# Optimization experiments

Hardware: AMD Instinct MI355X
Metric: run time of the kernel (lower is better)

## Reference

```python
import jax, jax.numpy as jnp
import numpy as np
import math

D = 128          # cfg.hiden_features_size
P0, P1 = 32, 32  # cfg.patch_size
T = 1.0          # default forward arg t


def _temporal_pe():
    # pe_k[i, :] = cat_j [sin(arg(t,i,j)), cos(arg(t,i,j))], i in [0,P1), j in [0,P0//2)
    i = jnp.arange(P1, dtype=jnp.float32)[:, None]          # [P1, 1]
    j = jnp.arange(P0 // 2, dtype=jnp.float32)[None, :]     # [1, P0//2]
    arg = T * jnp.pi * i / (1000.0 ** (2.0 * j / D))         # [P1, P0//2]
    pe = jnp.stack([jnp.sin(arg), jnp.cos(arg)], axis=-1)    # [P1, P0//2, 2]
    return pe.reshape(P1, P0)                                # [P1, P0]


def setup_inputs() -> dict:
    key = jax.random.key(0)
    kx, kw, kb = jax.random.split(key, 3)
    N, S = 128, P0 * P1
    x = jax.random.normal(kx, (N, S, D), dtype=jnp.float32)
    W = jax.random.normal(kw, (3 * D, D), dtype=jnp.float32) * (1.0 / math.sqrt(D))
    b = jax.random.normal(kb, (3 * D,), dtype=jnp.float32) * 0.01
    return {"x": x, "W": W, "b": b}


def reference(x, W, b):
    N, S, d = x.shape  # S = P0*P1, d = D
    # temporal positional encoding: multiply in spatial layout [N, P0, P1, d]
    pe = _temporal_pe()                                  # [P1, P0] (broadcast over x's [P0, P1])
    xs = x.reshape(N, P0, P1, d) * pe[None, :, :, None]
    xs = xs.reshape(N, S, d)
    # fused qkv projection: Linear(d, 3d)
    h = jnp.einsum('nsd,fd->nsf', xs, W) + b             # [N, S, 3d]
    # quirky split: view(N, S*d, 3) interleaves features in groups of 3
    qkv = h.reshape(N, S * d, 3)
    q, k, v = qkv[..., 0], qkv[..., 1], qkv[..., 2]      # each [N, S*d]
    # attention over the batch dimension: scores are [N, N]
    scores = (q @ k.T) / math.sqrt(d)
    attn = jax.nn.softmax(scores, axis=-1)
    return attn @ v                                      # [N, S*d]
```

## Files before the change

kernel.cpp:

```cpp
#include <hip/hip_runtime.h>
#include <math.h>

#define N_   128
#define S_   1024
#define D_   128
#define SD_  (S_ * D_)

#define WSP_PLANE 49152
#define NREP 16
#define SB   2
#define GRID_SC (S_ / SB)
#define QKP  36

typedef __attribute__((ext_vector_type(8))) short bf16x8;
typedef __attribute__((ext_vector_type(4))) short bf16x4;
typedef __attribute__((ext_vector_type(4))) float f32x4;
#define MFMA16 __builtin_amdgcn_mfma_f32_16x16x32_bf16

__device__ __forceinline__ float pe_scale(int s) {
    int i = s >> 5;
    int c = s & 31;
    double rexp = pow(1000.0, -(double)(c & ~1) / 128.0);
    double arg = M_PI * (double)i * rexp;
    return (float)((c & 1) ? cos(arg) : sin(arg));
}

__device__ __forceinline__ unsigned short bf16_rn(float f) {
    unsigned int u = __float_as_uint(f);
    u += 0x7fff + ((u >> 16) & 1);
    return (unsigned short)(u >> 16);
}
__device__ __forceinline__ float bf16_f(unsigned short h) {
    return __uint_as_float(((unsigned int)h) << 16);
}
__device__ __forceinline__ void split2(float f, unsigned short& h, unsigned short& l) {
    h = bf16_rn(f);
    l = bf16_rn(f - bf16_f(h));
}

__device__ __forceinline__ void load_split8(const float* p, float scale,
                                            bf16x8& hi, bf16x8& lo) {
    float4 u0 = *(const float4*)(p);
    float4 u1 = *(const float4*)(p + 4);
    unsigned short h[8], l[8];
    split2(u0.x * scale, h[0], l[0]); split2(u0.y * scale, h[1], l[1]);
    split2(u0.z * scale, h[2], l[2]); split2(u0.w * scale, h[3], l[3]);
    split2(u1.x * scale, h[4], l[4]); split2(u1.y * scale, h[5], l[5]);
    split2(u1.z * scale, h[6], l[6]); split2(u1.w * scale, h[7], l[7]);
    hi = bf16x8{(short)h[0],(short)h[1],(short)h[2],(short)h[3],
                (short)h[4],(short)h[5],(short)h[6],(short)h[7]};
    lo = bf16x8{(short)l[0],(short)l[1],(short)l[2],(short)l[3],
                (short)l[4],(short)l[5],(short)l[6],(short)l[7]};
}

__global__ __launch_bounds__(256) void k_prep(const float* __restrict__ W,
                                              unsigned short* __restrict__ Wsp,
                                              float* __restrict__ peT) {
    const int idx = blockIdx.x * 256 + threadIdx.x;
    if (idx < S_) peT[idx] = pe_scale(idx);
    const int rg = idx >> 7;
    const int d  = idx & 127;
    const int p  = rg % 3;
    const int r  = rg / 3;
    const int rc = r >> 5, m = r & 31;
    const int ks = d >> 5, quad = (d >> 3) & 3, j = d & 7;
    unsigned short h, l;
    split2(W[idx], h, l);
    const size_t off = (size_t)((((p * 4 + rc) * 4 + ks) * 4 + quad) * 32 + m) * 8 + j;
    Wsp[off] = h;
    Wsp[off + WSP_PLANE] = l;
}

__global__ __launch_bounds__(256, 2) void k_scores(const float* __restrict__ x,
                                                   const unsigned short* __restrict__ Wsp,
                                                   const float* __restrict__ b,
                                                   const float* __restrict__ peT,
                                                   float* __restrict__ sc,
                                                   int store_mode) {
    __shared__ unsigned short qk[2][4][128 * QKP];
    __shared__ float bl[384];

    const int t    = threadIdx.x;
    const int lane = t & 63;
    const int wv   = t >> 6;
    const int lid  = lane & 15;
    const int quad = lane >> 4;

    if (t < 128) { bl[t] = b[t]; bl[t + 128] = b[t + 128]; bl[t + 256] = b[t + 256]; }
    __syncthreads();

    const f32x4 fzero = {0.f, 0.f, 0.f, 0.f};
    f32x4 sacc[2][8];
#pragma unroll
    for (int i = 0; i < 2; ++i)
#pragma unroll
        for (int j = 0; j < 8; ++j) sacc[i][j] = fzero;

    for (int ss = 0; ss < SB; ++ss) {
        const int s = blockIdx.x * SB + ss;
        const float ps = peT[s];

        bf16x8 xh[2][4], xl[2][4];
#pragma unroll
        for (int nt = 0; nt < 2; ++nt) {
            const int row = (wv * 2 + nt) * 16 + lid;
            const float* xp = x + (size_t)row * SD_ + (size_t)s * D_;
#pragma unroll
            for (int ks = 0; ks < 4; ++ks)
                load_split8(xp + ks * 32 + quad * 8, ps, xh[nt][ks], xl[nt][ks]);
        }

        for (int rc = 0; rc < 4; ++rc) {
            const int buf = rc & 1;
            for (int p = 0; p < 2; ++p) {
                f32x4 pacc[2][2];
                pacc[0][0] = fzero; pacc[0][1] = fzero;
                pacc[1][0] = fzero; pacc[1][1] = fzero;
#pragma unroll
                for (int ks = 0; ks < 4; ++ks) {
                    const unsigned short* wb =
                        Wsp + (size_t)(((p * 4 + rc) * 4 + ks) * 4 + quad) * 256;
                    bf16x8 wh[2], wl[2];
#pragma unroll
                    for (int mt = 0; mt < 2; ++mt) {
                        wh[mt] = *(const bf16x8*)(wb + (mt * 16 + lid) * 8);
                        wl[mt] = *(const bf16x8*)(wb + WSP_PLANE + (mt * 16 + lid) * 8);
                    }
#pragma unroll
                    for (int mt = 0; mt < 2; ++mt)
#pragma unroll
                        for (int nt = 0; nt < 2; ++nt) {
                            pacc[mt][nt] = MFMA16(wh[mt], xh[nt][ks], pacc[mt][nt], 0, 0, 0);
                            pacc[mt][nt] = MFMA16(wh[mt], xl[nt][ks], pacc[mt][nt], 0, 0, 0);
                            pacc[mt][nt] = MFMA16(wl[mt], xh[nt][ks], pacc[mt][nt], 0, 0, 0);
                        }
                }
#pragma unroll
                for (int mt = 0; mt < 2; ++mt)
#pragma unroll
                    for (int nt = 0; nt < 2; ++nt) {
                        const int n = (wv * 2 + nt) * 16 + lid;
                        unsigned short hh[4], ll[4];
#pragma unroll
                        for (int r = 0; r < 4; ++r) {
                            const int rg = rc * 32 + mt * 16 + quad * 4 + r;
                            float qv = pacc[mt][nt][r] + bl[3 * rg + p];
                            split2(qv, hh[r], ll[r]);
                        }
                        bf16x4 hv = {(short)hh[0], (short)hh[1], (short)hh[2], (short)hh[3]};
                        bf16x4 lv = {(short)ll[0], (short)ll[1], (short)ll[2], (short)ll[3]};
                        *(bf16x4*)&qk[buf][p * 2 + 0][n * QKP + mt * 16 + quad * 4] = hv;
                        *(bf16x4*)&qk[buf][p * 2 + 1][n * QKP + mt * 16 + quad * 4] = lv;
                    }
            }
            __syncthreads();
            {
                bf16x8 qh[2], ql[2];
#pragma unroll
                for (int mt = 0; mt < 2; ++mt) {
                    const int row = wv * 32 + mt * 16 + lid;
                    qh[mt] = *(const bf16x8*)&qk[buf][0][row * QKP + quad * 8];
                    ql[mt] = *(const bf16x8*)&qk[buf][1][row * QKP + quad * 8];
                }
#pragma unroll
                for (int ntp = 0; ntp < 8; ++ntp) {
                    const int row = ntp * 16 + lid;
                    bf16x8 kh = *(const bf16x8*)&qk[buf][2][row * QKP + quad * 8];
                    bf16x8 kl = *(const bf16x8*)&qk[buf][3][row * QKP + quad * 8];
#pragma unroll
                    for (int mt = 0; mt < 2; ++mt) {
                        sacc[mt][ntp] = MFMA16(qh[mt], kh, sacc[mt][ntp], 0, 0, 0);
                        sacc[mt][ntp] = MFMA16(qh[mt], kl, sacc[mt][ntp], 0, 0, 0);
                        sacc[mt][ntp] = MFMA16(ql[mt], kh, sacc[mt][ntp], 0, 0, 0);
                    }
                }
            }
        }
    }

    float* rep = sc + (store_mode ? (size_t)blockIdx.x * (N_ * N_)
                                  : (size_t)(blockIdx.x & (NREP - 1)) * (N_ * N_));
#pragma unroll
    for (int mt = 0; mt < 2; ++mt)
#pragma unroll
        for (int ntp = 0; ntp < 8; ++ntp)
#pragma unroll
            for (int r = 0; r < 4; ++r) {
                const int n  = wv * 32 + mt * 16 + quad * 4 + r;
                const int np = ntp * 16 + lid;
                if (store_mode) rep[n * N_ + np] = sacc[mt][ntp][r];
                else            atomicAdd(&rep[n * N_ + np], sacc[mt][ntp][r]);
            }
}

__global__ __launch_bounds__(1024) void k_softmax(const float* __restrict__ sc, int R,
                                                  unsigned short* __restrict__ att2) {
    const int n  = blockIdx.x;
    const int t  = threadIdx.x;
    const int rg = t >> 5;
    const int c4 = (t & 31) * 4;

    float4 a = {0.f, 0.f, 0.f, 0.f};
    for (int rep = rg; rep < R; rep += 32) {
        const float4 p = *(const float4*)&sc[(size_t)rep * (N_ * N_) + n * N_ + c4];
        a.x += p.x; a.y += p.y; a.z += p.z; a.w += p.w;
    }
    __shared__ float tmp[32][128];
    *(float4*)&tmp[rg][c4] = a;
    __syncthreads();

    __shared__ float red[2];
    __shared__ float red2[2];

    float v = 0.f;
    if (t < 128) {
#pragma unroll
        for (int g = 0; g < 32; ++g) v += tmp[g][t];
        v *= 0.08838834764831845f;
    }

    float m = v;
#pragma unroll
    for (int o = 32; o > 0; o >>= 1) m = fmaxf(m, __shfl_xor(m, o));
    if (t < 128 && (t & 63) == 0) red[t >> 6] = m;
    __syncthreads();
    m = fmaxf(red[0], red[1]);

    float e = (t < 128) ? expf(v - m) : 0.f;
    float sum = e;
#pragma unroll
    for (int o = 32; o > 0; o >>= 1) sum += __shfl_xor(sum, o);
    if (t < 128 && (t & 63) == 0) red2[t >> 6] = sum;
    __syncthreads();
    sum = red2[0] + red2[1];

    if (t < 128) {
        const int ks = t >> 5, quad = (t >> 3) & 3, j = t & 7;
        att2[(size_t)(((ks * 4 + quad) * 128) + n) * 8 + j] = bf16_rn(e / sum);
    }
}

__global__ __launch_bounds__(256, 2) void k_out(const float* __restrict__ x,
                                                const unsigned short* __restrict__ Wsp,
                                                const float* __restrict__ b,
                                                const unsigned short* __restrict__ att2,
                                                const float* __restrict__ peT,
                                                float* __restrict__ out) {
    __shared__ unsigned short vT[128 * 136];
    __shared__ float bv[128];

    const int t    = threadIdx.x;
    const int lane = t & 63;
    const int wv   = t >> 6;
    const int lid  = lane & 15;
    const int quad = lane >> 4;
    const int s    = blockIdx.x;
    const float ps = peT[s];

    if (t < 128) bv[t] = b[3 * t + 2];
    __syncthreads();

    const f32x4 fzero = {0.f, 0.f, 0.f, 0.f};

    bf16x8 xh[2][4], xl[2][4];
#pragma unroll
    for (int mt = 0; mt < 2; ++mt) {
        const int row = (wv * 2 + mt) * 16 + lid;
        const float* xp = x + (size_t)row * SD_ + (size_t)s * D_;
#pragma unroll
        for (int ks = 0; ks < 4; ++ks)
            load_split8(xp + ks * 32 + quad * 8, ps, xh[mt][ks], xl[mt][ks]);
    }

    for (int rc = 0; rc < 4; ++rc) {
        f32x4 vacc[2][2];
        vacc[0][0] = fzero; vacc[0][1] = fzero; vacc[1][0] = fzero; vacc[1][1] = fzero;
#pragma unroll
        for (int ks = 0; ks < 4; ++ks) {
            const unsigned short* wb =
                Wsp + (size_t)(((2 * 4 + rc) * 4 + ks) * 4 + quad) * 256;
            bf16x8 wh[2], wl[2];
#pragma unroll
            for (int nt = 0; nt < 2; ++nt) {
                wh[nt] = *(const bf16x8*)(wb + (nt * 16 + lid) * 8);
                wl[nt] = *(const bf16x8*)(wb + WSP_PLANE + (nt * 16 + lid) * 8);
            }
#pragma unroll
            for (int mt = 0; mt < 2; ++mt)
#pragma unroll
                for (int nt = 0; nt < 2; ++nt) {
                    vacc[mt][nt] = MFMA16(xh[mt][ks], wh[nt], vacc[mt][nt], 0, 0, 0);
                    vacc[mt][nt] = MFMA16(xh[mt][ks], wl[nt], vacc[mt][nt], 0, 0, 0);
                    vacc[mt][nt] = MFMA16(xl[mt][ks], wh[nt], vacc[mt][nt], 0, 0, 0);
                }
        }
#pragma unroll
        for (int mt = 0; mt < 2; ++mt)
#pragma unroll
            for (int nt = 0; nt < 2; ++nt) {
                const int r = rc * 32 + nt * 16 + lid;
                const float bias = bv[r];
                unsigned short hh[4];
#pragma unroll
                for (int i = 0; i < 4; ++i) hh[i] = bf16_rn(vacc[mt][nt][i] + bias);
                bf16x4 hv = {(short)hh[0], (short)hh[1], (short)hh[2], (short)hh[3]};
                *(bf16x4*)&vT[r * 136 + (wv * 2 + mt) * 16 + quad * 4] = hv;
            }
    }
    __syncthreads();

    {
        f32x4 oacc[2][8];
#pragma unroll
        for (int i = 0; i < 2; ++i)
#pragma unroll
            for (int j = 0; j < 8; ++j) oacc[i][j] = fzero;
#pragma unroll
        for (int ks = 0; ks < 4; ++ks) {
            const int kofs = ks * 32 + quad * 8;
            bf16x8 a[2];
#pragma unroll
            for (int mt = 0; mt < 2; ++mt)
                a[mt] = *(const bf16x8*)&vT[((wv * 2 + mt) * 16 + lid) * 136 + kofs];
#pragma unroll
            for (int nt = 0; nt < 8; ++nt) {
                bf16x8 bb = *(const bf16x8*)&att2[(size_t)(((ks * 4 + quad) * 128) +
                                                           (nt * 16 + lid)) * 8];
#pragma unroll
                for (int mt = 0; mt < 2; ++mt)
                    oacc[mt][nt] = MFMA16(bb, a[mt], oacc[mt][nt], 0, 0, 0);
            }
        }
#pragma unroll
        for (int mt = 0; mt < 2; ++mt) {
            const int r = (wv * 2 + mt) * 16 + lid;
#pragma unroll
            for (int nt = 0; nt < 8; ++nt)
#pragma unroll
                for (int reg = 0; reg < 4; ++reg) {
                    const int n = nt * 16 + quad * 4 + reg;
                    out[(size_t)n * SD_ + (size_t)s * D_ + r] = oacc[mt][nt][reg];
                }
        }
    }
}

extern "C" void kernel_launch(void* const* d_in, const int* in_sizes, int n_in,
                              void* d_out, int out_size, void* d_ws, size_t ws_size,
                              hipStream_t stream) {
    const float* x = (const float*)d_in[0];
    const float* W = (const float*)d_in[1];
    const float* b = (const float*)d_in[2];
    float* out = (float*)d_out;

    const size_t store_bytes = (size_t)GRID_SC * N_ * N_ * sizeof(float);
    const size_t rep_bytes   = (size_t)NREP * N_ * N_ * sizeof(float);
    const size_t tail_bytes  = (size_t)N_ * N_ * sizeof(unsigned short)
                             + (size_t)2 * WSP_PLANE * sizeof(unsigned short)
                             + (size_t)S_ * sizeof(float);
    const int store_mode = (ws_size >= store_bytes + tail_bytes) ? 1 : 0;
    const size_t sc_bytes = store_mode ? store_bytes : rep_bytes;

    float* scores        = (float*)d_ws;
    unsigned short* att2 = (unsigned short*)((char*)d_ws + sc_bytes);
    unsigned short* Wsp  = att2 + N_ * N_;
    float* peT           = (float*)(Wsp + 2 * WSP_PLANE);

    if (!store_mode)
        hipMemsetAsync(scores, 0, sc_bytes, stream);

    hipLaunchKernelGGL(k_prep,    dim3(192),     dim3(256),  0, stream, W, Wsp, peT);
    hipLaunchKernelGGL(k_scores,  dim3(GRID_SC), dim3(256),  0, stream, x, Wsp, b, peT,
                       scores, store_mode);
    hipLaunchKernelGGL(k_softmax, dim3(N_),      dim3(1024), 0, stream, scores,
                       store_mode ? GRID_SC : NREP, att2);
    hipLaunchKernelGGL(k_out,     dim3(1024),    dim3(256),  0, stream, x, Wsp, b, att2,
                       peT, out);
}
```

Baseline: 205.9 us.

## Single-buffer qk tile, raise occupancy to 4 blocks, allow one s per block

Removes the LDS double buffer for q/k tiles and adds a trailing barrier, halving shared memory so launch bounds can request 4 blocks per CU for k_scores and k_out. Makes the s-per-block count a runtime parameter and picks 1 when the workspace fits 1024 partial score matrices, doubling the grid. This costs an extra barrier per rc step, more register pressure under the tighter bound, and a larger partial-score reduction in softmax (1024 slices instead of 512).

```diff
diff --git a/kernel.cpp b/kernel.cpp
--- a/kernel.cpp
+++ b/kernel.cpp
@@ -8,8 +8,6 @@
 
 #define WSP_PLANE 49152
 #define NREP 16
-#define SB   2
-#define GRID_SC (S_ / SB)
 #define QKP  36
 
 typedef __attribute__((ext_vector_type(8))) short bf16x8;
@@ -71,13 +69,13 @@
     Wsp[off + WSP_PLANE] = l;
 }
 
-__global__ __launch_bounds__(256, 2) void k_scores(const float* __restrict__ x,
+__global__ __launch_bounds__(256, 4) void k_scores(const float* __restrict__ x,
                                                    const unsigned short* __restrict__ Wsp,
                                                    const float* __restrict__ b,
                                                    const float* __restrict__ peT,
                                                    float* __restrict__ sc,
-                                                   int store_mode) {
-    __shared__ unsigned short qk[2][4][128 * QKP];
+                                                   int store_mode, int sb) {
+    __shared__ unsigned short qk[4][128 * QKP];
     __shared__ float bl[384];
 
     const int t    = threadIdx.x;
@@ -96,8 +94,8 @@
 #pragma unroll
         for (int j = 0; j < 8; ++j) sacc[i][j] = fzero;
 
-    for (int ss = 0; ss < SB; ++ss) {
-        const int s = blockIdx.x * SB + ss;
+    for (int ss = 0; ss < sb; ++ss) {
+        const int s = blockIdx.x * sb + ss;
         const float ps = peT[s];
 
         bf16x8 xh[2][4], xl[2][4];
@@ -111,7 +109,6 @@
         }
 
         for (int rc = 0; rc < 4; ++rc) {
-            const int buf = rc & 1;
             for (int p = 0; p < 2; ++p) {
                 f32x4 pacc[2][2];
                 pacc[0][0] = fzero; pacc[0][1] = fzero;
@@ -149,8 +146,8 @@
                         }
                         bf16x4 hv = {(short)hh[0], (short)hh[1], (short)hh[2], (short)hh[3]};
                         bf16x4 lv = {(short)ll[0], (short)ll[1], (short)ll[2], (short)ll[3]};
-                        *(bf16x4*)&qk[buf][p * 2 + 0][n * QKP + mt * 16 + quad * 4] = hv;
-                        *(bf16x4*)&qk[buf][p * 2 + 1][n * QKP + mt * 16 + quad * 4] = lv;
+                        *(bf16x4*)&qk[p * 2 + 0][n * QKP + mt * 16 + quad * 4] = hv;
+                        *(bf16x4*)&qk[p * 2 + 1][n * QKP + mt * 16 + quad * 4] = lv;
                     }
             }
             __syncthreads();
@@ -159,14 +156,14 @@
 #pragma unroll
                 for (int mt = 0; mt < 2; ++mt) {
                     const int row = wv * 32 + mt * 16 + lid;
-                    qh[mt] = *(const bf16x8*)&qk[buf][0][row * QKP + quad * 8];
-                    ql[mt] = *(const bf16x8*)&qk[buf][1][row * QKP + quad * 8];
+                    qh[mt] = *(const bf16x8*)&qk[0][row * QKP + quad * 8];
+                    ql[mt] = *(const bf16x8*)&qk[1][row * QKP + quad * 8];
                 }
 #pragma unroll
                 for (int ntp = 0; ntp < 8; ++ntp) {
                     const int row = ntp * 16 + lid;
-                    bf16x8 kh = *(const bf16x8*)&qk[buf][2][row * QKP + quad * 8];
-                    bf16x8 kl = *(const bf16x8*)&qk[buf][3][row * QKP + quad * 8];
+                    bf16x8 kh = *(const bf16x8*)&qk[2][row * QKP + quad * 8];
+                    bf16x8 kl = *(const bf16x8*)&qk[3][row * QKP + quad * 8];
 #pragma unroll
                     for (int mt = 0; mt < 2; ++mt) {
                         sacc[mt][ntp] = MFMA16(qh[mt], kh, sacc[mt][ntp], 0, 0, 0);
@@ -175,6 +172,7 @@
                     }
                 }
             }
+            __syncthreads();
         }
     }
 
@@ -240,7 +238,7 @@
     }
 }
 
-__global__ __launch_bounds__(256, 2) void k_out(const float* __restrict__ x,
+__global__ __launch_bounds__(256, 4) void k_out(const float* __restrict__ x,
                                                 const unsigned short* __restrict__ Wsp,
                                                 const float* __restrict__ b,
                                                 const unsigned short* __restrict__ att2,
@@ -353,13 +351,18 @@
     const float* b = (const float*)d_in[2];
     float* out = (float*)d_out;
 
-    const size_t store_bytes = (size_t)GRID_SC * N_ * N_ * sizeof(float);
-    const size_t rep_bytes   = (size_t)NREP * N_ * N_ * sizeof(float);
     const size_t tail_bytes  = (size_t)N_ * N_ * sizeof(unsigned short)
                              + (size_t)2 * WSP_PLANE * sizeof(unsigned short)
                              + (size_t)S_ * sizeof(float);
-    const int store_mode = (ws_size >= store_bytes + tail_bytes) ? 1 : 0;
-    const size_t sc_bytes = store_mode ? store_bytes : rep_bytes;
+    const size_t sb1_bytes = (size_t)1024 * N_ * N_ * sizeof(float);
+    const size_t sb2_bytes = (size_t)512  * N_ * N_ * sizeof(float);
+    const size_t rep_bytes = (size_t)NREP * N_ * N_ * sizeof(float);
+
+    int sb, grid_sc, store_mode;
+    size_t sc_bytes;
+    if (ws_size >= sb1_bytes + tail_bytes)      { sb = 1; grid_sc = 1024; store_mode = 1; sc_bytes = sb1_bytes; }
+    else if (ws_size >= sb2_bytes + tail_bytes) { sb = 2; grid_sc = 512;  store_mode = 1; sc_bytes = sb2_bytes; }
+    else                                        { sb = 2; grid_sc = 512;  store_mode = 0; sc_bytes = rep_bytes; }
 
     float* scores        = (float*)d_ws;
     unsigned short* att2 = (unsigned short*)((char*)d_ws + sc_bytes);
@@ -370,10 +373,10 @@
         hipMemsetAsync(scores, 0, sc_bytes, stream);
 
     hipLaunchKernelGGL(k_prep,    dim3(192),     dim3(256),  0, stream, W, Wsp, peT);
-    hipLaunchKernelGGL(k_scores,  dim3(GRID_SC), dim3(256),  0, stream, x, Wsp, b, peT,
-                       scores, store_mode);
+    hipLaunchKernelGGL(k_scores,  dim3(grid_sc), dim3(256),  0, stream, x, Wsp, b, peT,
+                       scores, store_mode, sb);
     hipLaunchKernelGGL(k_softmax, dim3(N_),      dim3(1024), 0, stream, scores,
-                       store_mode ? GRID_SC : NREP, att2);
+                       store_mode ? grid_sc : NREP, att2);
     hipLaunchKernelGGL(k_out,     dim3(1024),    dim3(256),  0, stream, x, Wsp, b, att2,
                        peT, out);
 }
```

Measured after the change: 316.7 us. +53.8%, slower.
